# Kernel optimization log

Measured on AMD Instinct MI355X. Metric: run time of the kernel, lower is better.

## Reference

```python
import jax, jax.numpy as jnp
import numpy as np

B, S, D = 2, 2048, 1024
E, K, F = 8, 2, 4 * 1024  # num_experts, top_k, fc_rate*embed_dim
T = B * S


def setup_inputs() -> dict:
    key = jax.random.key(0)
    ks = jax.random.split(key, 8)
    w = lambda k, shape: jax.random.normal(k, shape, jnp.float32) * 0.02
    return {
        "hidden_states": jax.random.normal(ks[0], (B, S, D), jnp.float32),
        "noise": jax.random.normal(ks[1], (T, E), jnp.float32),  # randn_like in router
        "Wg": w(ks[2], (D, E)), "bg": jnp.zeros((E,), jnp.float32),
        "Wn": w(ks[3], (D, E)), "bn": jnp.zeros((E,), jnp.float32),
        "W1": w(ks[4], (E, D, F)), "b1": jnp.zeros((E, F), jnp.float32),
        "W2": w(ks[5], (E, F, D)), "b2": jnp.zeros((E, D), jnp.float32),
    }


def reference(hidden_states, noise, Wg, bg, Wn, bn, W1, b1, W2, b2):
    b, s, d = hidden_states.shape
    x = hidden_states.reshape(-1, d)  # [T, D]

    # --- NoisyTopkRouter ---
    gate_logits = x @ Wg + bg                        # [T, E]
    noise_logits = x @ Wn + bn                       # [T, E]
    noisy_logits = gate_logits + noise * jax.nn.softplus(noise_logits)
    rw = jax.nn.softmax(noisy_logits.astype(jnp.float32), axis=-1)
    top_w, top_i = jax.lax.top_k(rw, K)              # [T, K]
    top_w = top_w / top_w.sum(-1, keepdims=True)
    top_w = top_w.astype(x.dtype)

    # Dense per-token combine coefficients: coef[t,e] = sum_k top_w[t,k]*[top_i[t,k]==e]
    tok = jnp.arange(x.shape[0])[:, None]
    coef = jnp.zeros((x.shape[0], E), x.dtype).at[tok, top_i].add(top_w)  # [T, E]

    # --- Experts: Linear -> GELU(exact) -> Linear (dropout = identity, eval mode) ---
    h = jax.nn.gelu(jnp.einsum('td,edf->tef', x, W1) + b1, approximate=False)  # [T,E,F]
    y = jnp.einsum('tef,efd->ted', h, W2) + b2                                  # [T,E,D]
    out = jnp.einsum('ted,te->td', y, coef)                                     # [T,D]

    return out.reshape(b, s, d), noisy_logits, gate_logits
```

## Files before the change

kernel.cpp:

```cpp
#include <hip/hip_runtime.h>
#include <hip/hip_bf16.h>

#define T_TOK 4096
#define D_DIM 1024
#define E_NUM 8
#define F_DIM 4096
#define NPAIR 8192

#define BM 128
#define BN 128
#define BK 64

typedef float f32x4 __attribute__((ext_vector_type(4)));
typedef __bf16 bf16x8 __attribute__((ext_vector_type(8)));
typedef unsigned short u16x8 __attribute__((ext_vector_type(8)));

__device__ __forceinline__ unsigned short f2bf(float f) {
    unsigned int u = __float_as_uint(f);
    u += 0x7fffu + ((u >> 16) & 1u);
    return (unsigned short)(u >> 16);
}

typedef const __attribute__((address_space(1))) void GV;
typedef __attribute__((address_space(3))) void LV;

__device__ __forceinline__ void load_lds16(const void* g, void* l) {
    __builtin_amdgcn_global_load_lds((GV*)g, (LV*)l, 16, 0, 0);
}

__global__ __launch_bounds__(256) void router_kernel(
    const float* __restrict__ x, const float* __restrict__ noise,
    const float* __restrict__ Wg, const float* __restrict__ bg,
    const float* __restrict__ Wn, const float* __restrict__ bn,
    float* __restrict__ out_noisy, float* __restrict__ out_gate,
    int* __restrict__ tk_idx, float* __restrict__ tk_w)
{
    int lane = threadIdx.x & 63;
    int t = blockIdx.x * 4 + (threadIdx.x >> 6);
    const float* xr = x + (size_t)t * D_DIM;

    float ag[E_NUM] = {}, an[E_NUM] = {};
    for (int it = 0; it < D_DIM / 64; ++it) {
        int d = it * 64 + lane;
        float xv = xr[d];
        float4 g0 = *(const float4*)(Wg + (size_t)d * E_NUM);
        float4 g1 = *(const float4*)(Wg + (size_t)d * E_NUM + 4);
        float4 m0 = *(const float4*)(Wn + (size_t)d * E_NUM);
        float4 m1 = *(const float4*)(Wn + (size_t)d * E_NUM + 4);
        ag[0] += xv * g0.x; ag[1] += xv * g0.y; ag[2] += xv * g0.z; ag[3] += xv * g0.w;
        ag[4] += xv * g1.x; ag[5] += xv * g1.y; ag[6] += xv * g1.z; ag[7] += xv * g1.w;
        an[0] += xv * m0.x; an[1] += xv * m0.y; an[2] += xv * m0.z; an[3] += xv * m0.w;
        an[4] += xv * m1.x; an[5] += xv * m1.y; an[6] += xv * m1.z; an[7] += xv * m1.w;
    }
    #pragma unroll
    for (int off = 32; off > 0; off >>= 1) {
        #pragma unroll
        for (int e = 0; e < E_NUM; ++e) {
            ag[e] += __shfl_xor(ag[e], off);
            an[e] += __shfl_xor(an[e], off);
        }
    }
    if (lane == 0) {
        float nz[E_NUM];
        #pragma unroll
        for (int e = 0; e < E_NUM; ++e) {
            float g = ag[e] + bg[e];
            float nn = an[e] + bn[e];
            float sp = fmaxf(nn, 0.f) + log1pf(expf(-fabsf(nn)));
            float z = g + noise[(size_t)t * E_NUM + e] * sp;
            out_gate[(size_t)t * E_NUM + e] = g;
            out_noisy[(size_t)t * E_NUM + e] = z;
            nz[e] = z;
        }
        int e0 = 0;
        #pragma unroll
        for (int e = 1; e < E_NUM; ++e) if (nz[e] > nz[e0]) e0 = e;
        int e1 = (e0 == 0) ? 1 : 0;
        #pragma unroll
        for (int e = 0; e < E_NUM; ++e) if (e != e0 && nz[e] > nz[e1]) e1 = e;
        float b = expf(nz[e1] - nz[e0]);
        float w0 = 1.f / (1.f + b);
        float w1 = b / (1.f + b);
        tk_idx[t * 2] = e0;  tk_idx[t * 2 + 1] = e1;
        tk_w[t * 2] = w0;    tk_w[t * 2 + 1] = w1;
    }
}

__global__ __launch_bounds__(256) void scan_scatter_kernel(
    const int* __restrict__ tk_idx,
    int* __restrict__ perm, int* __restrict__ meta)
{
    __shared__ int cnt[256][E_NUM];
    __shared__ int soff[E_NUM];
    int tid = threadIdx.x;
    const int PPT = NPAIR / 256;
    int p0 = tid * PPT;

    int c[E_NUM] = {};
    for (int i = 0; i < PPT; ++i) c[tk_idx[p0 + i]]++;
    #pragma unroll
    for (int e = 0; e < E_NUM; ++e) cnt[tid][e] = c[e];
    __syncthreads();

    if (tid < E_NUM) {
        int s = 0;
        for (int j = 0; j < 256; ++j) { int v = cnt[j][tid]; cnt[j][tid] = s; s += v; }
        soff[tid] = s;
    }
    __syncthreads();

    if (tid == 0) {
        int off = 0, nt = 0;
        for (int e = 0; e < E_NUM; ++e) {
            int ce = soff[e];
            meta[1 + e] = off;
            meta[9 + e] = ce;
            for (int j = 0; j < ce; j += BM) {
                meta[32 + nt]  = e;
                meta[160 + nt] = off + j;
                meta[288 + nt] = off + ce;
                nt++;
            }
            off += ce;
        }
        meta[0] = nt;
    }
    __syncthreads();
    if (tid < E_NUM) soff[tid] = meta[1 + tid];
    __syncthreads();

    int pos[E_NUM];
    #pragma unroll
    for (int e = 0; e < E_NUM; ++e) pos[e] = soff[e] + cnt[tid][e];
    for (int i = 0; i < PPT; ++i) {
        int e = tk_idx[p0 + i];
        perm[pos[e]++] = p0 + i;
    }
}

__global__ __launch_bounds__(256) void convert_x_kernel(
    const float* __restrict__ x, unsigned short* __restrict__ xb)
{
    size_t i = ((size_t)blockIdx.x * 256 + threadIdx.x) * 8;
    float4 a = *(const float4*)(x + i);
    float4 b = *(const float4*)(x + i + 4);
    u16x8 o;
    o[0] = f2bf(a.x); o[1] = f2bf(a.y); o[2] = f2bf(a.z); o[3] = f2bf(a.w);
    o[4] = f2bf(b.x); o[5] = f2bf(b.y); o[6] = f2bf(b.z); o[7] = f2bf(b.w);
    *(u16x8*)(xb + i) = o;
}

__global__ __launch_bounds__(256) void transpose_kernel(
    const float* __restrict__ W, unsigned short* __restrict__ WT, int R, int C)
{
    __shared__ float tile[32][33];
    int e = blockIdx.z;
    int c0 = blockIdx.x * 32, r0 = blockIdx.y * 32;
    int tx = threadIdx.x & 31, ty = threadIdx.x >> 5;
    const float* src = W + (size_t)e * R * C;
    #pragma unroll
    for (int i = 0; i < 4; ++i)
        tile[ty + 8 * i][tx] = src[(size_t)(r0 + ty + 8 * i) * C + c0 + tx];
    __syncthreads();
    unsigned short* dst = WT + (size_t)e * C * R;
    #pragma unroll
    for (int i = 0; i < 4; ++i)
        dst[(size_t)(c0 + ty + 8 * i) * R + r0 + tx] = f2bf(tile[tx][ty + 8 * i]);
}

__global__ __launch_bounds__(256) void fc1_kernel(
    const unsigned short* __restrict__ xb,
    const unsigned short* __restrict__ W1T,
    const float* __restrict__ b1,
    const int* __restrict__ perm,
    const int* __restrict__ meta,
    unsigned short* __restrict__ h)
{
    int tile = blockIdx.x;
    if (tile >= meta[0]) return;
    int e    = meta[32 + tile];
    int rs   = meta[160 + tile];
    int rend = meta[288 + tile];
    int n0 = blockIdx.y * BN;

    __shared__ unsigned short As[BM][BK];
    __shared__ unsigned short Bs[BN][BK];

    int tid = threadIdx.x, lane = tid & 63, wv = tid >> 6;
    int wm = (wv >> 1) * 64, wn = (wv & 1) * 64;

    const unsigned short* asrc[4];
    #pragma unroll
    for (int i = 0; i < 4; ++i) {
        int q = tid + i * 256;
        int r = q >> 3, c = q & 7;
        int pos = rs + r; if (pos >= NPAIR) pos = NPAIR - 1;
        int t = perm[pos] >> 1;
        asrc[i] = xb + (size_t)t * D_DIM + c * 8;
    }
    const unsigned short* bbase = W1T + ((size_t)e * F_DIM + n0 + wv * 32 + (lane >> 3)) * D_DIM
                                + (lane & 7) * 8;

    f32x4 acc[4][4] = {};

    for (int k0 = 0; k0 < D_DIM; k0 += BK) {
        __syncthreads();
        #pragma unroll
        for (int i = 0; i < 4; ++i) {
            int q = tid + i * 256;
            int r = q >> 3, c = q & 7;
            *(u16x8*)&As[r][c * 8] = *(const u16x8*)(asrc[i] + k0);
        }
        #pragma unroll
        for (int j = 0; j < 4; ++j) {
            load_lds16(bbase + (size_t)j * 8 * D_DIM + k0, &Bs[wv * 32 + j * 8][0]);
        }
        __syncthreads();
        #pragma unroll
        for (int kk = 0; kk < BK; kk += 32) {
            bf16x8 af[4], bf[4];
            #pragma unroll
            for (int m = 0; m < 4; ++m)
                af[m] = *(const bf16x8*)&As[wm + m * 16 + (lane & 15)][kk + (lane >> 4) * 8];
            #pragma unroll
            for (int n = 0; n < 4; ++n)
                bf[n] = *(const bf16x8*)&Bs[wn + n * 16 + (lane & 15)][kk + (lane >> 4) * 8];
            #pragma unroll
            for (int m = 0; m < 4; ++m)
                #pragma unroll
                for (int n = 0; n < 4; ++n)
                    acc[m][n] = __builtin_amdgcn_mfma_f32_16x16x32_bf16(af[m], bf[n], acc[m][n], 0, 0, 0);
        }
    }

    #pragma unroll
    for (int m = 0; m < 4; ++m) {
        #pragma unroll
        for (int j = 0; j < 4; ++j) {
            int r = wm + m * 16 + (lane >> 4) * 4 + j;
            int pos = rs + r;
            if (pos >= rend) continue;
            #pragma unroll
            for (int n = 0; n < 4; ++n) {
                int col = n0 + wn + n * 16 + (lane & 15);
                float v = acc[m][n][j] + b1[e * F_DIM + col];
                v = 0.5f * v * (1.f + erff(v * 0.70710678118654752f));
                h[(size_t)pos * F_DIM + col] = f2bf(v);
            }
        }
    }
}

__global__ __launch_bounds__(256) void fc2_kernel(
    const unsigned short* __restrict__ h,
    const unsigned short* __restrict__ W2T,
    const float* __restrict__ b2,
    const int* __restrict__ perm,
    const float* __restrict__ tk_w,
    const int* __restrict__ meta,
    float* __restrict__ out)
{
    int tile = blockIdx.x;
    if (tile >= meta[0]) return;
    int e    = meta[32 + tile];
    int rs   = meta[160 + tile];
    int rend = meta[288 + tile];
    int n0 = blockIdx.y * BN;

    __shared__ unsigned short As[BM][BK];
    __shared__ unsigned short Bs[BN][BK];

    int tid = threadIdx.x, lane = tid & 63, wv = tid >> 6;
    int wm = (wv >> 1) * 64, wn = (wv & 1) * 64;

    f32x4 acc[4][4] = {};

    for (int k0 = 0; k0 < F_DIM; k0 += BK) {
        __syncthreads();
        #pragma unroll
        for (int j = 0; j < 4; ++j) {
            int r = wv * 32 + j * 8 + (lane >> 3);
            int pos = rs + r; if (pos >= NPAIR) pos = NPAIR - 1;
            const unsigned short* g = h + (size_t)pos * F_DIM + k0 + (lane & 7) * 8;
            load_lds16(g, &As[wv * 32 + j * 8][0]);
        }
        #pragma unroll
        for (int j = 0; j < 4; ++j) {
            const unsigned short* g = W2T + ((size_t)e * D_DIM + n0 + wv * 32 + j * 8 + (lane >> 3)) * F_DIM
                                    + k0 + (lane & 7) * 8;
            load_lds16(g, &Bs[wv * 32 + j * 8][0]);
        }
        __syncthreads();
        #pragma unroll
        for (int kk = 0; kk < BK; kk += 32) {
            bf16x8 af[4], bf[4];
            #pragma unroll
            for (int m = 0; m < 4; ++m)
                af[m] = *(const bf16x8*)&As[wm + m * 16 + (lane & 15)][kk + (lane >> 4) * 8];
            #pragma unroll
            for (int n = 0; n < 4; ++n)
                bf[n] = *(const bf16x8*)&Bs[wn + n * 16 + (lane & 15)][kk + (lane >> 4) * 8];
            #pragma unroll
            for (int m = 0; m < 4; ++m)
                #pragma unroll
                for (int n = 0; n < 4; ++n)
                    acc[m][n] = __builtin_amdgcn_mfma_f32_16x16x32_bf16(af[m], bf[n], acc[m][n], 0, 0, 0);
        }
    }

    #pragma unroll
    for (int m = 0; m < 4; ++m) {
        #pragma unroll
        for (int j = 0; j < 4; ++j) {
            int r = wm + m * 16 + (lane >> 4) * 4 + j;
            int pos = rs + r;
            if (pos >= rend) continue;
            int pr = perm[pos];
            int t = pr >> 1;
            float w = tk_w[pr];
            #pragma unroll
            for (int n = 0; n < 4; ++n) {
                int col = n0 + wn + n * 16 + (lane & 15);
                float v = (acc[m][n][j] + b2[e * D_DIM + col]) * w;
                atomicAdd(&out[(size_t)t * D_DIM + col], v);
            }
        }
    }
}

extern "C" void kernel_launch(void* const* d_in, const int* in_sizes, int n_in,
                              void* d_out, int out_size, void* d_ws, size_t ws_size,
                              hipStream_t stream)
{
    const float* x     = (const float*)d_in[0];
    const float* noise = (const float*)d_in[1];
    const float* Wg    = (const float*)d_in[2];
    const float* bg    = (const float*)d_in[3];
    const float* Wn    = (const float*)d_in[4];
    const float* bn    = (const float*)d_in[5];
    const float* W1    = (const float*)d_in[6];
    const float* b1    = (const float*)d_in[7];
    const float* W2    = (const float*)d_in[8];
    const float* b2    = (const float*)d_in[9];

    float* out       = (float*)d_out;
    float* out_noisy = out + (size_t)T_TOK * D_DIM;
    float* out_gate  = out_noisy + (size_t)T_TOK * E_NUM;

    char* ws = (char*)d_ws;
    int*   tk_idx = (int*)ws;
    float* tk_w   = (float*)(ws + 32768);
    int*   perm   = (int*)(ws + 65536);
    int*   meta   = (int*)(ws + 98304);
    size_t off = 131072;
    unsigned short* xb   = (unsigned short*)(ws + off); off += (size_t)T_TOK * D_DIM * 2;
    unsigned short* W1T  = (unsigned short*)(ws + off); off += (size_t)E_NUM * F_DIM * D_DIM * 2;
    unsigned short* W2T  = (unsigned short*)(ws + off); off += (size_t)E_NUM * D_DIM * F_DIM * 2;
    unsigned short* hbuf = (unsigned short*)(ws + off); off += (size_t)NPAIR * F_DIM * 2;

    hipMemsetAsync(d_out, 0, (size_t)out_size * sizeof(float), stream);

    convert_x_kernel<<<(T_TOK * D_DIM) / (256 * 8), 256, 0, stream>>>(x, xb);
    transpose_kernel<<<dim3(F_DIM / 32, D_DIM / 32, E_NUM), 256, 0, stream>>>(W1, W1T, D_DIM, F_DIM);
    transpose_kernel<<<dim3(D_DIM / 32, F_DIM / 32, E_NUM), 256, 0, stream>>>(W2, W2T, F_DIM, D_DIM);
    router_kernel<<<T_TOK / 4, 256, 0, stream>>>(x, noise, Wg, bg, Wn, bn,
                                                 out_noisy, out_gate, tk_idx, tk_w);
    scan_scatter_kernel<<<1, 256, 0, stream>>>(tk_idx, perm, meta);

    fc1_kernel<<<dim3(71, F_DIM / BN), 256, 0, stream>>>(xb, W1T, b1, perm, meta, hbuf);
    fc2_kernel<<<dim3(71, D_DIM / BN), 256, 0, stream>>>(hbuf, W2T, b2, perm, tk_w, meta, out);
}
```

Baseline: 568.8 us.

## Split-K the FC2 expert GEMM and use direct-to-LDS loads for gathered rows

Result: slower. 634.5 us (+11.6%).

```diff
diff --git a/kernel.cpp b/kernel.cpp
--- a/kernel.cpp
+++ b/kernel.cpp
@@ -10,6 +10,7 @@
 #define BM 128
 #define BN 128
 #define BK 64
+#define KSPLIT 4
 
 typedef float f32x4 __attribute__((ext_vector_type(4)));
 typedef __bf16 bf16x8 __attribute__((ext_vector_type(8)));
@@ -198,6 +199,7 @@
         int t = perm[pos] >> 1;
         asrc[i] = xb + (size_t)t * D_DIM + c * 8;
     }
+    unsigned short* Asf = &As[0][0];
     const unsigned short* bbase = W1T + ((size_t)e * F_DIM + n0 + wv * 32 + (lane >> 3)) * D_DIM
                                 + (lane & 7) * 8;
 
@@ -206,15 +208,11 @@
     for (int k0 = 0; k0 < D_DIM; k0 += BK) {
         __syncthreads();
         #pragma unroll
-        for (int i = 0; i < 4; ++i) {
-            int q = tid + i * 256;
-            int r = q >> 3, c = q & 7;
-            *(u16x8*)&As[r][c * 8] = *(const u16x8*)(asrc[i] + k0);
-        }
-        #pragma unroll
-        for (int j = 0; j < 4; ++j) {
+        for (int i = 0; i < 4; ++i)
+            load_lds16(asrc[i] + k0, Asf + ((size_t)wv * 64 + i * 256) * 8);
+        #pragma unroll
+        for (int j = 0; j < 4; ++j)
             load_lds16(bbase + (size_t)j * 8 * D_DIM + k0, &Bs[wv * 32 + j * 8][0]);
-        }
         __syncthreads();
         #pragma unroll
         for (int kk = 0; kk < BK; kk += 32) {
@@ -266,6 +264,9 @@
     int rs   = meta[160 + tile];
     int rend = meta[288 + tile];
     int n0 = blockIdx.y * BN;
+    int ks   = blockIdx.z;
+    int kbeg = ks * (F_DIM / KSPLIT);
+    int kend = kbeg + (F_DIM / KSPLIT);
 
     __shared__ unsigned short As[BM][BK];
     __shared__ unsigned short Bs[BN][BK];
@@ -273,23 +274,28 @@
     int tid = threadIdx.x, lane = tid & 63, wv = tid >> 6;
     int wm = (wv >> 1) * 64, wn = (wv & 1) * 64;
 
+    const unsigned short* asrc[4];
+    #pragma unroll
+    for (int i = 0; i < 4; ++i) {
+        int q = tid + i * 256;
+        int r = q >> 3, c = q & 7;
+        int pos = rs + r; if (pos >= NPAIR) pos = NPAIR - 1;
+        asrc[i] = h + (size_t)pos * F_DIM + c * 8;
+    }
+    unsigned short* Asf = &As[0][0];
+    const unsigned short* bbase = W2T + ((size_t)e * D_DIM + n0 + wv * 32 + (lane >> 3)) * F_DIM
+                                + (lane & 7) * 8;
+
     f32x4 acc[4][4] = {};
 
-    for (int k0 = 0; k0 < F_DIM; k0 += BK) {
+    for (int k0 = kbeg; k0 < kend; k0 += BK) {
         __syncthreads();
         #pragma unroll
-        for (int j = 0; j < 4; ++j) {
-            int r = wv * 32 + j * 8 + (lane >> 3);
-            int pos = rs + r; if (pos >= NPAIR) pos = NPAIR - 1;
-            const unsigned short* g = h + (size_t)pos * F_DIM + k0 + (lane & 7) * 8;
-            load_lds16(g, &As[wv * 32 + j * 8][0]);
-        }
-        #pragma unroll
-        for (int j = 0; j < 4; ++j) {
-            const unsigned short* g = W2T + ((size_t)e * D_DIM + n0 + wv * 32 + j * 8 + (lane >> 3)) * F_DIM
-                                    + k0 + (lane & 7) * 8;
-            load_lds16(g, &Bs[wv * 32 + j * 8][0]);
-        }
+        for (int i = 0; i < 4; ++i)
+            load_lds16(asrc[i] + k0, Asf + ((size_t)wv * 64 + i * 256) * 8);
+        #pragma unroll
+        for (int j = 0; j < 4; ++j)
+            load_lds16(bbase + (size_t)j * 8 * F_DIM + k0, &Bs[wv * 32 + j * 8][0]);
         __syncthreads();
         #pragma unroll
         for (int kk = 0; kk < BK; kk += 32) {
@@ -321,7 +327,8 @@
             #pragma unroll
             for (int n = 0; n < 4; ++n) {
                 int col = n0 + wn + n * 16 + (lane & 15);
-                float v = (acc[m][n][j] + b2[e * D_DIM + col]) * w;
+                float base = (ks == 0) ? b2[e * D_DIM + col] : 0.f;
+                float v = (acc[m][n][j] + base) * w;
                 atomicAdd(&out[(size_t)t * D_DIM + col], v);
             }
         }
@@ -360,13 +367,13 @@
 
     hipMemsetAsync(d_out, 0, (size_t)out_size * sizeof(float), stream);
 
+    router_kernel<<<T_TOK / 4, 256, 0, stream>>>(x, noise, Wg, bg, Wn, bn,
+                                                 out_noisy, out_gate, tk_idx, tk_w);
+    scan_scatter_kernel<<<1, 256, 0, stream>>>(tk_idx, perm, meta);
     convert_x_kernel<<<(T_TOK * D_DIM) / (256 * 8), 256, 0, stream>>>(x, xb);
     transpose_kernel<<<dim3(F_DIM / 32, D_DIM / 32, E_NUM), 256, 0, stream>>>(W1, W1T, D_DIM, F_DIM);
     transpose_kernel<<<dim3(D_DIM / 32, F_DIM / 32, E_NUM), 256, 0, stream>>>(W2, W2T, F_DIM, D_DIM);
-    router_kernel<<<T_TOK / 4, 256, 0, stream>>>(x, noise, Wg, bg, Wn, bn,
-                                                 out_noisy, out_gate, tk_idx, tk_w);
-    scan_scatter_kernel<<<1, 256, 0, stream>>>(tk_idx, perm, meta);
 
     fc1_kernel<<<dim3(71, F_DIM / BN), 256, 0, stream>>>(xb, W1T, b1, perm, meta, hbuf);
-    fc2_kernel<<<dim3(71, D_DIM / BN), 256, 0, stream>>>(hbuf, W2T, b2, perm, tk_w, meta, out);
-}
+    fc2_kernel<<<dim3(71, D_DIM / BN, KSPLIT), 256, 0, stream>>>(hbuf, W2T, b2, perm, tk_w, meta, out);
+}
```

## Double-buffer LDS in expert GEMMs with XOR swizzle and XCD-aware tile remap

Applied to the files above, without the earlier changes.

Result: faster. 505.9 us (-11.1%).

```diff
diff --git a/kernel.cpp b/kernel.cpp
--- a/kernel.cpp
+++ b/kernel.cpp
@@ -26,6 +26,11 @@
 
 __device__ __forceinline__ void load_lds16(const void* g, void* l) {
     __builtin_amdgcn_global_load_lds((GV*)g, (LV*)l, 16, 0, 0);
+}
+
+__device__ __forceinline__ bf16x8 lds_frag(const unsigned short* S, int row, int cs) {
+    int byte = row * (BK * 2) + ((cs * 2) ^ ((row & 7) << 4));
+    return *(const bf16x8*)((const char*)S + byte);
 }
 
 __global__ __launch_bounds__(256) void router_kernel(
@@ -176,62 +181,78 @@
     const int* __restrict__ meta,
     unsigned short* __restrict__ h)
 {
-    int tile = blockIdx.x;
+    const int nwg = 71 * (F_DIM / BN);
+    const int cpx = nwg >> 3;
+    int bid = blockIdx.x;
+    int wg = (bid & 7) * cpx + (bid >> 3);
+    int tile = wg >> 5;
+    int n0 = (wg & 31) * BN;
     if (tile >= meta[0]) return;
     int e    = meta[32 + tile];
     int rs   = meta[160 + tile];
     int rend = meta[288 + tile];
-    int n0 = blockIdx.y * BN;
-
-    __shared__ unsigned short As[BM][BK];
-    __shared__ unsigned short Bs[BN][BK];
+
+    __shared__ __align__(16) unsigned short As[2][BM * BK];
+    __shared__ __align__(16) unsigned short Bs[2][BN * BK];
 
     int tid = threadIdx.x, lane = tid & 63, wv = tid >> 6;
     int wm = (wv >> 1) * 64, wn = (wv & 1) * 64;
+    int csw = ((tid & 7) ^ ((tid >> 3) & 7)) * 8;
 
     const unsigned short* asrc[4];
     #pragma unroll
     for (int i = 0; i < 4; ++i) {
         int q = tid + i * 256;
-        int r = q >> 3, c = q & 7;
-        int pos = rs + r; if (pos >= NPAIR) pos = NPAIR - 1;
+        int pos = rs + (q >> 3); if (pos >= NPAIR) pos = NPAIR - 1;
         int t = perm[pos] >> 1;
-        asrc[i] = xb + (size_t)t * D_DIM + c * 8;
-    }
-    const unsigned short* bbase = W1T + ((size_t)e * F_DIM + n0 + wv * 32 + (lane >> 3)) * D_DIM
-                                + (lane & 7) * 8;
+        asrc[i] = xb + (size_t)t * D_DIM + csw;
+    }
+    const unsigned short* bbase = W1T + ((size_t)e * F_DIM + n0 + wv * 32 + (lane >> 3)) * D_DIM + csw;
 
     f32x4 acc[4][4] = {};
 
-    for (int k0 = 0; k0 < D_DIM; k0 += BK) {
-        __syncthreads();
-        #pragma unroll
-        for (int i = 0; i < 4; ++i) {
-            int q = tid + i * 256;
-            int r = q >> 3, c = q & 7;
-            *(u16x8*)&As[r][c * 8] = *(const u16x8*)(asrc[i] + k0);
-        }
-        #pragma unroll
-        for (int j = 0; j < 4; ++j) {
-            load_lds16(bbase + (size_t)j * 8 * D_DIM + k0, &Bs[wv * 32 + j * 8][0]);
-        }
-        __syncthreads();
+#define STAGE1(k0, b) do { \
+    _Pragma("unroll") \
+    for (int i_ = 0; i_ < 4; ++i_) \
+        load_lds16(asrc[i_] + (k0), &As[b][(wv * 64 + i_ * 256) * 8]); \
+    _Pragma("unroll") \
+    for (int j_ = 0; j_ < 4; ++j_) \
+        load_lds16(bbase + (size_t)(j_ * 8) * D_DIM + (k0), &Bs[b][(wv * 32 + j_ * 8) * BK]); \
+} while (0)
+
+    STAGE1(0, 0);
+    const int NT = D_DIM / BK;
+    #pragma unroll 2
+    for (int t = 0; t < NT; ++t) {
+        int cur = t & 1;
+        if (t + 1 < NT) {
+            STAGE1((t + 1) * BK, cur ^ 1);
+            asm volatile("s_waitcnt vmcnt(8)" ::: "memory");
+        } else {
+            asm volatile("s_waitcnt vmcnt(0)" ::: "memory");
+        }
+        __builtin_amdgcn_s_barrier();
+        const unsigned short* A = As[cur];
+        const unsigned short* B = Bs[cur];
         #pragma unroll
         for (int kk = 0; kk < BK; kk += 32) {
             bf16x8 af[4], bf[4];
             #pragma unroll
             for (int m = 0; m < 4; ++m)
-                af[m] = *(const bf16x8*)&As[wm + m * 16 + (lane & 15)][kk + (lane >> 4) * 8];
+                af[m] = lds_frag(A, wm + m * 16 + (lane & 15), kk + (lane >> 4) * 8);
             #pragma unroll
             for (int n = 0; n < 4; ++n)
-                bf[n] = *(const bf16x8*)&Bs[wn + n * 16 + (lane & 15)][kk + (lane >> 4) * 8];
+                bf[n] = lds_frag(B, wn + n * 16 + (lane & 15), kk + (lane >> 4) * 8);
             #pragma unroll
             for (int m = 0; m < 4; ++m)
                 #pragma unroll
                 for (int n = 0; n < 4; ++n)
                     acc[m][n] = __builtin_amdgcn_mfma_f32_16x16x32_bf16(af[m], bf[n], acc[m][n], 0, 0, 0);
         }
-    }
+        asm volatile("s_waitcnt lgkmcnt(0)" ::: "memory");
+        __builtin_amdgcn_s_barrier();
+    }
+#undef STAGE1
 
     #pragma unroll
     for (int m = 0; m < 4; ++m) {
@@ -260,53 +281,77 @@
     const int* __restrict__ meta,
     float* __restrict__ out)
 {
-    int tile = blockIdx.x;
+    const int nwg = 71 * (D_DIM / BN);
+    const int cpx = nwg >> 3;
+    int bid = blockIdx.x;
+    int wg = (bid & 7) * cpx + (bid >> 3);
+    int tile = wg >> 3;
+    int n0 = (wg & 7) * BN;
     if (tile >= meta[0]) return;
     int e    = meta[32 + tile];
     int rs   = meta[160 + tile];
     int rend = meta[288 + tile];
-    int n0 = blockIdx.y * BN;
-
-    __shared__ unsigned short As[BM][BK];
-    __shared__ unsigned short Bs[BN][BK];
+
+    __shared__ __align__(16) unsigned short As[2][BM * BK];
+    __shared__ __align__(16) unsigned short Bs[2][BN * BK];
 
     int tid = threadIdx.x, lane = tid & 63, wv = tid >> 6;
     int wm = (wv >> 1) * 64, wn = (wv & 1) * 64;
+    int csw = ((tid & 7) ^ ((tid >> 3) & 7)) * 8;
+
+    const unsigned short* asrc[4];
+    #pragma unroll
+    for (int i = 0; i < 4; ++i) {
+        int q = tid + i * 256;
+        int pos = rs + (q >> 3); if (pos >= NPAIR) pos = NPAIR - 1;
+        asrc[i] = h + (size_t)pos * F_DIM + csw;
+    }
+    const unsigned short* bbase = W2T + ((size_t)e * D_DIM + n0 + wv * 32 + (lane >> 3)) * F_DIM + csw;
 
     f32x4 acc[4][4] = {};
 
-    for (int k0 = 0; k0 < F_DIM; k0 += BK) {
-        __syncthreads();
-        #pragma unroll
-        for (int j = 0; j < 4; ++j) {
-            int r = wv * 32 + j * 8 + (lane >> 3);
-            int pos = rs + r; if (pos >= NPAIR) pos = NPAIR - 1;
-            const unsigned short* g = h + (size_t)pos * F_DIM + k0 + (lane & 7) * 8;
-            load_lds16(g, &As[wv * 32 + j * 8][0]);
-        }
-        #pragma unroll
-        for (int j = 0; j < 4; ++j) {
-            const unsigned short* g = W2T + ((size_t)e * D_DIM + n0 + wv * 32 + j * 8 + (lane >> 3)) * F_DIM
-                                    + k0 + (lane & 7) * 8;
-            load_lds16(g, &Bs[wv * 32 + j * 8][0]);
-        }
-        __syncthreads();
+#define STAGE2(k0, b) do { \
+    _Pragma("unroll") \
+    for (int i_ = 0; i_ < 4; ++i_) \
+        load_lds16(asrc[i_] + (k0), &As[b][(wv * 64 + i_ * 256) * 8]); \
+    _Pragma("unroll") \
+    for (int j_ = 0; j_ < 4; ++j_) \
+        load_lds16(bbase + (size_t)(j_ * 8) * F_DIM + (k0), &Bs[b][(wv * 32 + j_ * 8) * BK]); \
+} while (0)
+
+    STAGE2(0, 0);
+    const int NT = F_DIM / BK;
+    #pragma unroll 2
+    for (int t = 0; t < NT; ++t) {
+        int cur = t & 1;
+        if (t + 1 < NT) {
+            STAGE2((t + 1) * BK, cur ^ 1);
+            asm volatile("s_waitcnt vmcnt(8)" ::: "memory");
+        } else {
+            asm volatile("s_waitcnt vmcnt(0)" ::: "memory");
+        }
+        __builtin_amdgcn_s_barrier();
+        const unsigned short* A = As[cur];
+        const unsigned short* B = Bs[cur];
         #pragma unroll
         for (int kk = 0; kk < BK; kk += 32) {
             bf16x8 af[4], bf[4];
             #pragma unroll
             for (int m = 0; m < 4; ++m)
-                af[m] = *(const bf16x8*)&As[wm + m * 16 + (lane & 15)][kk + (lane >> 4) * 8];
+                af[m] = lds_frag(A, wm + m * 16 + (lane & 15), kk + (lane >> 4) * 8);
             #pragma unroll
             for (int n = 0; n < 4; ++n)
-                bf[n] = *(const bf16x8*)&Bs[wn + n * 16 + (lane & 15)][kk + (lane >> 4) * 8];
+                bf[n] = lds_frag(B, wn + n * 16 + (lane & 15), kk + (lane >> 4) * 8);
             #pragma unroll
             for (int m = 0; m < 4; ++m)
                 #pragma unroll
                 for (int n = 0; n < 4; ++n)
                     acc[m][n] = __builtin_amdgcn_mfma_f32_16x16x32_bf16(af[m], bf[n], acc[m][n], 0, 0, 0);
         }
-    }
+        asm volatile("s_waitcnt lgkmcnt(0)" ::: "memory");
+        __builtin_amdgcn_s_barrier();
+    }
+#undef STAGE2
 
     #pragma unroll
     for (int m = 0; m < 4; ++m) {
@@ -360,13 +405,13 @@
 
     hipMemsetAsync(d_out, 0, (size_t)out_size * sizeof(float), stream);
 
+    router_kernel<<<T_TOK / 4, 256, 0, stream>>>(x, noise, Wg, bg, Wn, bn,
+                                                 out_noisy, out_gate, tk_idx, tk_w);
+    scan_scatter_kernel<<<1, 256, 0, stream>>>(tk_idx, perm, meta);
     convert_x_kernel<<<(T_TOK * D_DIM) / (256 * 8), 256, 0, stream>>>(x, xb);
     transpose_kernel<<<dim3(F_DIM / 32, D_DIM / 32, E_NUM), 256, 0, stream>>>(W1, W1T, D_DIM, F_DIM);
     transpose_kernel<<<dim3(D_DIM / 32, F_DIM / 32, E_NUM), 256, 0, stream>>>(W2, W2T, F_DIM, D_DIM);
-    router_kernel<<<T_TOK / 4, 256, 0, stream>>>(x, noise, Wg, bg, Wn, bn,
-                                                 out_noisy, out_gate, tk_idx, tk_w);
-    scan_scatter_kernel<<<1, 256, 0, stream>>>(tk_idx, perm, meta);
-
-    fc1_kernel<<<dim3(71, F_DIM / BN), 256, 0, stream>>>(xb, W1T, b1, perm, meta, hbuf);
-    fc2_kernel<<<dim3(71, D_DIM / BN), 256, 0, stream>>>(hbuf, W2T, b2, perm, tk_w, meta, out);
-}
+
+    fc1_kernel<<<71 * (F_DIM / BN), 256, 0, stream>>>(xb, W1T, b1, perm, meta, hbuf);
+    fc2_kernel<<<71 * (D_DIM / BN), 256, 0, stream>>>(hbuf, W2T, b2, perm, tk_w, meta, out);
+}
```

## Pre-pack operands into MFMA fragment layout and drop LDS staging in expert GEMMs

Applied to the files above, without the earlier changes.

New measurement: 640.5 us. 1.13x slower.

```diff
diff --git a/kernel.cpp b/kernel.cpp
--- a/kernel.cpp
+++ b/kernel.cpp
@@ -7,9 +7,8 @@
 #define F_DIM 4096
 #define NPAIR 8192
 
-#define BM 128
-#define BN 128
-#define BK 64
+#define NTMAX 39
+#define NMID (NTMAX * 2)
 
 typedef float f32x4 __attribute__((ext_vector_type(4)));
 typedef __bf16 bf16x8 __attribute__((ext_vector_type(8)));
@@ -19,13 +18,6 @@
     unsigned int u = __float_as_uint(f);
     u += 0x7fffu + ((u >> 16) & 1u);
     return (unsigned short)(u >> 16);
-}
-
-typedef const __attribute__((address_space(1))) void GV;
-typedef __attribute__((address_space(3))) void LV;
-
-__device__ __forceinline__ void load_lds16(const void* g, void* l) {
-    __builtin_amdgcn_global_load_lds((GV*)g, (LV*)l, 16, 0, 0);
 }
 
 __global__ __launch_bounds__(256) void router_kernel(
@@ -115,7 +107,7 @@
             int ce = soff[e];
             meta[1 + e] = off;
             meta[9 + e] = ce;
-            for (int j = 0; j < ce; j += BM) {
+            for (int j = 0; j < ce; j += 256) {
                 meta[32 + nt]  = e;
                 meta[160 + nt] = off + j;
                 meta[288 + nt] = off + ce;
@@ -138,191 +130,157 @@
     }
 }
 
-__global__ __launch_bounds__(256) void convert_x_kernel(
-    const float* __restrict__ x, unsigned short* __restrict__ xb)
-{
-    size_t i = ((size_t)blockIdx.x * 256 + threadIdx.x) * 8;
-    float4 a = *(const float4*)(x + i);
-    float4 b = *(const float4*)(x + i + 4);
-    u16x8 o;
-    o[0] = f2bf(a.x); o[1] = f2bf(a.y); o[2] = f2bf(a.z); o[3] = f2bf(a.w);
-    o[4] = f2bf(b.x); o[5] = f2bf(b.y); o[6] = f2bf(b.z); o[7] = f2bf(b.w);
-    *(u16x8*)(xb + i) = o;
-}
-
-__global__ __launch_bounds__(256) void transpose_kernel(
-    const float* __restrict__ W, unsigned short* __restrict__ WT, int R, int C)
-{
-    __shared__ float tile[32][33];
-    int e = blockIdx.z;
-    int c0 = blockIdx.x * 32, r0 = blockIdx.y * 32;
-    int tx = threadIdx.x & 31, ty = threadIdx.x >> 5;
-    const float* src = W + (size_t)e * R * C;
-    #pragma unroll
-    for (int i = 0; i < 4; ++i)
-        tile[ty + 8 * i][tx] = src[(size_t)(r0 + ty + 8 * i) * C + c0 + tx];
-    __syncthreads();
-    unsigned short* dst = WT + (size_t)e * C * R;
-    #pragma unroll
-    for (int i = 0; i < 4; ++i)
-        dst[(size_t)(c0 + ty + 8 * i) * R + r0 + tx] = f2bf(tile[tx][ty + 8 * i]);
-}
-
-__global__ __launch_bounds__(256) void fc1_kernel(
-    const unsigned short* __restrict__ xb,
-    const unsigned short* __restrict__ W1T,
-    const float* __restrict__ b1,
-    const int* __restrict__ perm,
-    const int* __restrict__ meta,
-    unsigned short* __restrict__ h)
+__global__ __launch_bounds__(256) void pack_x_kernel(
+    const float* __restrict__ x, const int* __restrict__ perm,
+    const int* __restrict__ meta, unsigned short* __restrict__ xg)
 {
     int tile = blockIdx.x;
     if (tile >= meta[0]) return;
-    int e    = meta[32 + tile];
-    int rs   = meta[160 + tile];
-    int rend = meta[288 + tile];
-    int n0 = blockIdx.y * BN;
-
-    __shared__ unsigned short As[BM][BK];
-    __shared__ unsigned short Bs[BN][BK];
-
-    int tid = threadIdx.x, lane = tid & 63, wv = tid >> 6;
+    int rs = meta[160 + tile];
+    int r = threadIdx.x;
+    int pos = rs + r; if (pos >= NPAIR) pos = NPAIR - 1;
+    int t = perm[pos] >> 1;
+    const float* xr = x + (size_t)t * D_DIM;
+    unsigned short* dst = xg + ((size_t)tile * 128) * 256 * 8;
+    for (int kb = 0; kb < 128; ++kb) {
+        float4 a = *(const float4*)(xr + kb * 8);
+        float4 b = *(const float4*)(xr + kb * 8 + 4);
+        u16x8 o;
+        o[0] = f2bf(a.x); o[1] = f2bf(a.y); o[2] = f2bf(a.z); o[3] = f2bf(a.w);
+        o[4] = f2bf(b.x); o[5] = f2bf(b.y); o[6] = f2bf(b.z); o[7] = f2bf(b.w);
+        *(u16x8*)(dst + ((size_t)kb * 256 + r) * 8) = o;
+    }
+}
+
+__global__ __launch_bounds__(256) void pack_w_kernel(
+    const float* __restrict__ W, unsigned short* __restrict__ WP, int R, int C)
+{
+    int e = blockIdx.z, kb = blockIdx.y;
+    int f = blockIdx.x * 256 + threadIdx.x;
+    const float* src = W + ((size_t)e * R + kb * 8) * C + f;
+    u16x8 o;
+    #pragma unroll
+    for (int i = 0; i < 8; ++i) o[i] = f2bf(src[(size_t)i * C]);
+    *(u16x8*)(WP + (((size_t)e * (R / 8) + kb) * C + f) * 8) = o;
+}
+
+__global__ __launch_bounds__(256, 4) void fc1_kernel(
+    const unsigned short* __restrict__ xg,
+    const unsigned short* __restrict__ W1P,
+    const float* __restrict__ b1,
+    const int* __restrict__ meta,
+    unsigned short* __restrict__ hP)
+{
+    int bid = blockIdx.x;
+    int n0i = bid / NMID, Mid = bid % NMID;
+    int tile = Mid >> 1, mhalf = Mid & 1;
+    if (tile >= meta[0]) return;
+    int e = meta[32 + tile], rs = meta[160 + tile], rend = meta[288 + tile];
+    int n0 = n0i * 128;
+
+    int lane = threadIdx.x & 63, wv = threadIdx.x >> 6;
     int wm = (wv >> 1) * 64, wn = (wv & 1) * 64;
-
-    const unsigned short* asrc[4];
-    #pragma unroll
-    for (int i = 0; i < 4; ++i) {
-        int q = tid + i * 256;
-        int r = q >> 3, c = q & 7;
-        int pos = rs + r; if (pos >= NPAIR) pos = NPAIR - 1;
-        int t = perm[pos] >> 1;
-        asrc[i] = xb + (size_t)t * D_DIM + c * 8;
-    }
-    const unsigned short* bbase = W1T + ((size_t)e * F_DIM + n0 + wv * 32 + (lane >> 3)) * D_DIM
-                                + (lane & 7) * 8;
+    int l15 = lane & 15, l16 = lane >> 4;
+
+    const bf16x8* ap = (const bf16x8*)xg + (size_t)tile * (128 * 256)
+                     + (size_t)l16 * 256 + (mhalf * 128 + wm + l15);
+    const bf16x8* bp = (const bf16x8*)W1P + (size_t)e * (128 * F_DIM)
+                     + (size_t)l16 * F_DIM + (n0 + wn + l15);
 
     f32x4 acc[4][4] = {};
-
-    for (int k0 = 0; k0 < D_DIM; k0 += BK) {
-        __syncthreads();
-        #pragma unroll
-        for (int i = 0; i < 4; ++i) {
-            int q = tid + i * 256;
-            int r = q >> 3, c = q & 7;
-            *(u16x8*)&As[r][c * 8] = *(const u16x8*)(asrc[i] + k0);
-        }
-        #pragma unroll
-        for (int j = 0; j < 4; ++j) {
-            load_lds16(bbase + (size_t)j * 8 * D_DIM + k0, &Bs[wv * 32 + j * 8][0]);
-        }
-        __syncthreads();
-        #pragma unroll
-        for (int kk = 0; kk < BK; kk += 32) {
-            bf16x8 af[4], bf[4];
-            #pragma unroll
-            for (int m = 0; m < 4; ++m)
-                af[m] = *(const bf16x8*)&As[wm + m * 16 + (lane & 15)][kk + (lane >> 4) * 8];
+    #pragma unroll 2
+    for (int t = 0; t < D_DIM / 32; ++t) {
+        bf16x8 af[4], bf[4];
+        #pragma unroll
+        for (int m = 0; m < 4; ++m) af[m] = ap[(size_t)t * 1024 + m * 16];
+        #pragma unroll
+        for (int n = 0; n < 4; ++n) bf[n] = bp[(size_t)t * 4 * F_DIM + n * 16];
+        __builtin_amdgcn_s_setprio(1);
+        #pragma unroll
+        for (int m = 0; m < 4; ++m)
             #pragma unroll
             for (int n = 0; n < 4; ++n)
-                bf[n] = *(const bf16x8*)&Bs[wn + n * 16 + (lane & 15)][kk + (lane >> 4) * 8];
-            #pragma unroll
-            for (int m = 0; m < 4; ++m)
-                #pragma unroll
-                for (int n = 0; n < 4; ++n)
-                    acc[m][n] = __builtin_amdgcn_mfma_f32_16x16x32_bf16(af[m], bf[n], acc[m][n], 0, 0, 0);
-        }
+                acc[m][n] = __builtin_amdgcn_mfma_f32_16x16x32_bf16(af[m], bf[n], acc[m][n], 0, 0, 0);
+        __builtin_amdgcn_s_setprio(0);
     }
 
     #pragma unroll
     for (int m = 0; m < 4; ++m) {
         #pragma unroll
         for (int j = 0; j < 4; ++j) {
-            int r = wm + m * 16 + (lane >> 4) * 4 + j;
-            int pos = rs + r;
-            if (pos >= rend) continue;
+            int r = mhalf * 128 + wm + m * 16 + l16 * 4 + j;
+            int p = rs + r;
+            if (p >= rend) continue;
             #pragma unroll
             for (int n = 0; n < 4; ++n) {
-                int col = n0 + wn + n * 16 + (lane & 15);
+                int col = n0 + wn + n * 16 + l15;
                 float v = acc[m][n][j] + b1[e * F_DIM + col];
                 v = 0.5f * v * (1.f + erff(v * 0.70710678118654752f));
-                h[(size_t)pos * F_DIM + col] = f2bf(v);
+                hP[(((size_t)tile * 512 + (col >> 3)) * 256 + r) * 8 + (col & 7)] = f2bf(v);
             }
         }
     }
 }
 
-__global__ __launch_bounds__(256) void fc2_kernel(
-    const unsigned short* __restrict__ h,
-    const unsigned short* __restrict__ W2T,
+__global__ __launch_bounds__(256, 4) void fc2_kernel(
+    const unsigned short* __restrict__ hP,
+    const unsigned short* __restrict__ W2P,
     const float* __restrict__ b2,
     const int* __restrict__ perm,
     const float* __restrict__ tk_w,
     const int* __restrict__ meta,
     float* __restrict__ out)
 {
-    int tile = blockIdx.x;
+    int bid = blockIdx.x;
+    int g = bid / NMID, Mid = bid % NMID;
+    int d0i = g >> 1, ks = g & 1;
+    int tile = Mid >> 1, mhalf = Mid & 1;
     if (tile >= meta[0]) return;
-    int e    = meta[32 + tile];
-    int rs   = meta[160 + tile];
-    int rend = meta[288 + tile];
-    int n0 = blockIdx.y * BN;
-
-    __shared__ unsigned short As[BM][BK];
-    __shared__ unsigned short Bs[BN][BK];
-
-    int tid = threadIdx.x, lane = tid & 63, wv = tid >> 6;
+    int e = meta[32 + tile], rs = meta[160 + tile], rend = meta[288 + tile];
+    int kb0 = ks * 256;
+
+    int lane = threadIdx.x & 63, wv = threadIdx.x >> 6;
     int wm = (wv >> 1) * 64, wn = (wv & 1) * 64;
+    int l15 = lane & 15, l16 = lane >> 4;
+
+    const bf16x8* ap = (const bf16x8*)hP + ((size_t)tile * 512 + kb0 + l16) * 256
+                     + (mhalf * 128 + wm + l15);
+    const bf16x8* bp = (const bf16x8*)W2P + ((size_t)e * 512 + kb0 + l16) * D_DIM
+                     + (d0i * 128 + wn + l15);
 
     f32x4 acc[4][4] = {};
-
-    for (int k0 = 0; k0 < F_DIM; k0 += BK) {
-        __syncthreads();
-        #pragma unroll
-        for (int j = 0; j < 4; ++j) {
-            int r = wv * 32 + j * 8 + (lane >> 3);
-            int pos = rs + r; if (pos >= NPAIR) pos = NPAIR - 1;
-            const unsigned short* g = h + (size_t)pos * F_DIM + k0 + (lane & 7) * 8;
-            load_lds16(g, &As[wv * 32 + j * 8][0]);
-        }
-        #pragma unroll
-        for (int j = 0; j < 4; ++j) {
-            const unsigned short* g = W2T + ((size_t)e * D_DIM + n0 + wv * 32 + j * 8 + (lane >> 3)) * F_DIM
-                                    + k0 + (lane & 7) * 8;
-            load_lds16(g, &Bs[wv * 32 + j * 8][0]);
-        }
-        __syncthreads();
-        #pragma unroll
-        for (int kk = 0; kk < BK; kk += 32) {
-            bf16x8 af[4], bf[4];
-            #pragma unroll
-            for (int m = 0; m < 4; ++m)
-                af[m] = *(const bf16x8*)&As[wm + m * 16 + (lane & 15)][kk + (lane >> 4) * 8];
+    #pragma unroll 2
+    for (int t = 0; t < 64; ++t) {
+        bf16x8 af[4], bf[4];
+        #pragma unroll
+        for (int m = 0; m < 4; ++m) af[m] = ap[(size_t)t * 1024 + m * 16];
+        #pragma unroll
+        for (int n = 0; n < 4; ++n) bf[n] = bp[(size_t)t * 4 * D_DIM + n * 16];
+        __builtin_amdgcn_s_setprio(1);
+        #pragma unroll
+        for (int m = 0; m < 4; ++m)
             #pragma unroll
             for (int n = 0; n < 4; ++n)
-                bf[n] = *(const bf16x8*)&Bs[wn + n * 16 + (lane & 15)][kk + (lane >> 4) * 8];
-            #pragma unroll
-            for (int m = 0; m < 4; ++m)
-                #pragma unroll
-                for (int n = 0; n < 4; ++n)
-                    acc[m][n] = __builtin_amdgcn_mfma_f32_16x16x32_bf16(af[m], bf[n], acc[m][n], 0, 0, 0);
-        }
+                acc[m][n] = __builtin_amdgcn_mfma_f32_16x16x32_bf16(af[m], bf[n], acc[m][n], 0, 0, 0);
+        __builtin_amdgcn_s_setprio(0);
     }
 
     #pragma unroll
     for (int m = 0; m < 4; ++m) {
         #pragma unroll
         for (int j = 0; j < 4; ++j) {
-            int r = wm + m * 16 + (lane >> 4) * 4 + j;
-            int pos = rs + r;
-            if (pos >= rend) continue;
-            int pr = perm[pos];
-            int t = pr >> 1;
+            int r = mhalf * 128 + wm + m * 16 + l16 * 4 + j;
+            int p = rs + r;
+            if (p >= rend) continue;
+            int pr = perm[p];
+            int t2 = pr >> 1;
             float w = tk_w[pr];
             #pragma unroll
             for (int n = 0; n < 4; ++n) {
-                int col = n0 + wn + n * 16 + (lane & 15);
-                float v = (acc[m][n][j] + b2[e * D_DIM + col]) * w;
-                atomicAdd(&out[(size_t)t * D_DIM + col], v);
+                int col = d0i * 128 + wn + n * 16 + l15;
+                float base = (ks == 0) ? b2[e * D_DIM + col] : 0.f;
+                float v = (acc[m][n][j] + base) * w;
+                atomicAdd(&out[(size_t)t2 * D_DIM + col], v);
             }
         }
     }
@@ -353,20 +311,20 @@
     int*   perm   = (int*)(ws + 65536);
     int*   meta   = (int*)(ws + 98304);
     size_t off = 131072;
-    unsigned short* xb   = (unsigned short*)(ws + off); off += (size_t)T_TOK * D_DIM * 2;
-    unsigned short* W1T  = (unsigned short*)(ws + off); off += (size_t)E_NUM * F_DIM * D_DIM * 2;
-    unsigned short* W2T  = (unsigned short*)(ws + off); off += (size_t)E_NUM * D_DIM * F_DIM * 2;
-    unsigned short* hbuf = (unsigned short*)(ws + off); off += (size_t)NPAIR * F_DIM * 2;
+    unsigned short* xg  = (unsigned short*)(ws + off); off += (size_t)NTMAX * 128 * 256 * 8 * 2;
+    unsigned short* W1P = (unsigned short*)(ws + off); off += (size_t)E_NUM * 128 * F_DIM * 8 * 2;
+    unsigned short* W2P = (unsigned short*)(ws + off); off += (size_t)E_NUM * 512 * D_DIM * 8 * 2;
+    unsigned short* hP  = (unsigned short*)(ws + off); off += (size_t)NTMAX * 512 * 256 * 8 * 2;
 
     hipMemsetAsync(d_out, 0, (size_t)out_size * sizeof(float), stream);
 
-    convert_x_kernel<<<(T_TOK * D_DIM) / (256 * 8), 256, 0, stream>>>(x, xb);
-    transpose_kernel<<<dim3(F_DIM / 32, D_DIM / 32, E_NUM), 256, 0, stream>>>(W1, W1T, D_DIM, F_DIM);
-    transpose_kernel<<<dim3(D_DIM / 32, F_DIM / 32, E_NUM), 256, 0, stream>>>(W2, W2T, F_DIM, D_DIM);
     router_kernel<<<T_TOK / 4, 256, 0, stream>>>(x, noise, Wg, bg, Wn, bn,
                                                  out_noisy, out_gate, tk_idx, tk_w);
     scan_scatter_kernel<<<1, 256, 0, stream>>>(tk_idx, perm, meta);
-
-    fc1_kernel<<<dim3(71, F_DIM / BN), 256, 0, stream>>>(xb, W1T, b1, perm, meta, hbuf);
-    fc2_kernel<<<dim3(71, D_DIM / BN), 256, 0, stream>>>(hbuf, W2T, b2, perm, tk_w, meta, out);
-}
+    pack_x_kernel<<<NTMAX, 256, 0, stream>>>(x, perm, meta, xg);
+    pack_w_kernel<<<dim3(D_DIM / 256, F_DIM / 8, E_NUM), 256, 0, stream>>>(W2, W2P, F_DIM, D_DIM);
+    pack_w_kernel<<<dim3(F_DIM / 256, D_DIM / 8, E_NUM), 256, 0, stream>>>(W1, W1P, D_DIM, F_DIM);
+
+    fc1_kernel<<<32 * NMID, 256, 0, stream>>>(xg, W1P, b1, meta, hP);
+    fc2_kernel<<<16 * NMID, 256, 0, stream>>>(hP, W2P, b2, perm, tk_w, meta, out);
+}
```
